# Optimization experiments

Hardware: AMD Instinct MI355X
Metric: run time of the kernel (lower is better)

Reference implementation:

```python
import jax, jax.numpy as jnp
import numpy as np

BIG = 10000000.0

def heaviside(x):
    return (jnp.tanh(BIG * x) + 1.0) * 0.5

def interception(Prec, PET, INSC):
    INSC = jnp.clip(INSC * 5.0, 0.5, 5.0)
    IMAX = jnp.maximum(jnp.minimum(INSC, PET), 0.0)
    INT = jnp.maximum(jnp.minimum(IMAX, Prec), 0.0)
    INR = jnp.maximum(Prec - INT, 0.0)
    return INT, INR

def soil_moisture_store(SMS1, SMSC):
    SMSC = jnp.clip(SMSC * 500.0, 50.0, 500.0)
    return jnp.maximum(jnp.minimum(SMS1, SMSC), 0.0)

def soil_fluxes(PET, INT, INR, COEFF, SQ, SMSC, SUB, CRAK, SMS1):
    COEFF = jnp.clip(COEFF * 400.0, 50.0, 400.0)
    SQ = jnp.clip(SQ * 6.0, 0.0, 6.0)
    SMSC = jnp.clip(SMSC * 500.0, 50.0, 500.0)
    SUB = jnp.clip(SUB, 0.0, 1.0)
    CRAK = jnp.clip(CRAK, 0.0, 1.0)
    cap = COEFF * jnp.exp(-SQ * SMS1 / SMSC)
    RMO = jnp.maximum(heaviside(cap - INR) * INR + heaviside(INR - cap) * cap, 0.0)
    IRUN = jnp.maximum(INR - RMO, 0.0)
    SRUN = jnp.maximum(SUB * (SMS1 / SMSC) * RMO, 0.0)
    REC = jnp.maximum(CRAK * (SMS1 / SMSC) * (RMO - SRUN), 0.0)
    SMF = jnp.maximum(RMO - SRUN - REC, 0.0)
    POT = jnp.maximum(PET - INT, 0.0)
    r = 10.0 * SMS1 / SMSC
    ETS = jnp.maximum(heaviside(r - POT) * POT + heaviside(POT - r) * r, 0.0)
    return RMO, IRUN, SRUN, REC, SMF, ETS

def recharge_calculation(SMS1, SMSC, REC, SMF, ETS):
    SMSC = jnp.clip(SMSC * 500.0, 50.0, 500.0)
    s = SMS1 + SMF - ETS
    RECnew = heaviside(s - SMSC) * (REC + s - SMSC) + heaviside(SMSC - s) * REC
    return jnp.maximum(RECnew, 0.0)

def groundwaterstore(GW1, RecK):
    RecK = jnp.clip(RecK * 0.3, 0.003, 0.3)
    return jnp.maximum(heaviside(GW1) * (RecK * GW1), 0.0)

def _forward(inputs, INSC, COEFF, SQ, SMSC, SUB, CRAK, RecK):
    B, T, _ = inputs.shape
    xs = jnp.transpose(inputs, (1, 0, 2))  # (T, B, 2)

    def step(carry, x):
        SMS1, GW1 = carry  # each (B, 1)
        Prec, PET = x[:, 0:1], x[:, 1:2]
        INT, INR = interception(Prec, PET, INSC)
        SMS1c = soil_moisture_store(SMS1, SMSC)
        RMO, IRUN, SRUN, REC, SMF, ETS = soil_fluxes(PET, INT, INR, COEFF, SQ, SMSC, SUB, CRAK, SMS1c)
        next_SMS = SMS1c + jnp.clip(SMF - ETS, -100000.0, 100000.0)
        RECnew = recharge_calculation(SMS1c, SMSC, REC, SMF, ETS)
        BAS = groundwaterstore(GW1, RecK)
        next_GW = GW1 + jnp.clip(RECnew - BAS, -100000.0, 100000.0)
        return (next_SMS, next_GW), jnp.concatenate([next_SMS, next_GW], axis=1)

    init = (jnp.zeros((B, 1), inputs.dtype), jnp.zeros((B, 1), inputs.dtype))
    _, outs = jax.lax.scan(step, init, xs)  # (T, B, 2)
    outs = jnp.transpose(outs, (1, 0, 2))   # (B, T, 2)
    outs = jnp.roll(outs, shift=1, axis=1)  # state at step t-1 (wrap like tf.roll)
    SMS1 = outs[:, :, 0:1]
    GW1 = outs[:, :, 1:2]
    Prec = inputs[:, :, 0:1]
    PET = inputs[:, :, 1:2]
    INT, INR = interception(Prec, PET, INSC)
    SMS1 = soil_moisture_store(SMS1, SMSC)
    RMO, IRUN, SRUN, REC, SMF, ETS = soil_fluxes(PET, INT, INR, COEFF, SQ, SMSC, SUB, CRAK, SMS1)
    RECnew = recharge_calculation(SMS1, SMSC, REC, SMF, ETS)
    BAS = groundwaterstore(GW1, RecK)
    DR = jnp.maximum(SRUN + IRUN, 0.0)
    GD = jnp.maximum(BAS, 0.0)
    Q = jnp.maximum(DR + GD, 0.0)
    return Q  # (B, T, 1)


def setup_inputs() -> dict:
    key = jax.random.key(0)
    k1, = jax.random.split(key, 1)
    B, T = 4096, 1024
    # Prec in [0, 20) mm/day, PET in [0, 8) mm/day
    u = jax.random.uniform(k1, (B, T, 2), dtype=jnp.float32)
    scale = jnp.array([20.0, 8.0], dtype=jnp.float32)
    inputs = u * scale
    p = lambda v: jnp.full((1,), v, dtype=jnp.float32)
    return {
        "inputs": inputs,
        "INSC": p(0.5), "COEFF": p(0.5), "SQ": p(0.5), "SMSC": p(0.5),
        "SUB": p(0.5), "CRAK": p(0.5), "RecK": p(0.5),
    }


def reference(inputs, INSC, COEFF, SQ, SMSC, SUB, CRAK, RecK):
    return _forward(inputs, INSC, COEFF, SQ, SMSC, SUB, CRAK, RecK)
```

## Files before the change

### kernel.cpp

```cpp
#include <hip/hip_runtime.h>
#include <hip/hip_bf16.h>
#include <math.h>


struct P {
    float INSC, COEFF, SMSC, RecK, k1, k2, k3, c2;
};

__device__ __forceinline__ P make_params(const float* pINSC, const float* pCOEFF,
                                         const float* pSQ,   const float* pSMSC,
                                         const float* pSUB,  const float* pCRAK,
                                         const float* pRecK) {
    P p;
    p.INSC  = fminf(fmaxf(pINSC[0]  * 5.0f,   0.5f),   5.0f);
    p.COEFF = fminf(fmaxf(pCOEFF[0] * 400.0f, 50.0f),  400.0f);
    float SQ = fminf(fmaxf(pSQ[0]   * 6.0f,   0.0f),   6.0f);
    p.SMSC  = fminf(fmaxf(pSMSC[0]  * 500.0f, 50.0f),  500.0f);
    float SUB  = fminf(fmaxf(pSUB[0],  0.0f), 1.0f);
    float CRAK = fminf(fmaxf(pCRAK[0], 0.0f), 1.0f);
    p.RecK  = fminf(fmaxf(pRecK[0]  * 0.3f,   0.003f), 0.3f);
    float inv = 1.0f / p.SMSC;
    p.k1 = SUB * inv;
    p.k2 = CRAK * inv;
    p.k3 = 10.0f * inv;
    p.c2 = (-SQ * inv) * 1.44269504088896340736f;
    return p;
}

__device__ __forceinline__ float step(float Prec, float PET, float& sms, float& gw, const P& p) {
    float INT   = fminf(fminf(p.INSC, PET), Prec);
    float INR   = Prec - INT;
    float POT   = PET - INT;
    float S     = fmaxf(fminf(sms, p.SMSC), 0.0f);
    float cap   = p.COEFF * exp2f(p.c2 * S);
    float RMO   = fminf(INR, cap);
    float IRUN  = INR - RMO;
    float SRUN  = (p.k1 * S) * RMO;
    float t2    = RMO - SRUN;
    float REC   = (p.k2 * S) * t2;
    float SMF   = t2 - REC;
    float ETS   = fminf(POT, p.k3 * S);
    float s2    = S + (SMF - ETS);
    float RECnew = REC + fmaxf(s2 - p.SMSC, 0.0f);
    float BAS   = p.RecK * gw;
    float Q     = (SRUN + IRUN) + BAS;
    sms = s2;
    gw  = gw + (RECnew - BAS);
    return Q;
}

__device__ __forceinline__ void stepw(float Prec, float PET, float& sms, float& gw, const P& p) {
    float INT   = fminf(fminf(p.INSC, PET), Prec);
    float INR   = Prec - INT;
    float POT   = PET - INT;
    float S     = fmaxf(fminf(sms, p.SMSC), 0.0f);
    float cap   = p.COEFF * exp2f(p.c2 * S);
    float RMO   = fminf(INR, cap);
    float SRUN  = (p.k1 * S) * RMO;
    float t2    = RMO - SRUN;
    float REC   = (p.k2 * S) * t2;
    float SMF   = t2 - REC;
    float ETS   = fminf(POT, p.k3 * S);
    float s2    = S + (SMF - ETS);
    float RECnew = REC + fmaxf(s2 - p.SMSC, 0.0f);
    float BAS   = p.RecK * gw;
    sms = s2;
    gw  = gw + (RECnew - BAS);
}

__device__ __forceinline__ void dstep(float Prec, float PET,
                                      float& slo, float& shi, float& gw, const P& p) {
    float INT = fminf(fminf(p.INSC, PET), Prec);
    float INR = Prec - INT;
    float POT = PET - INT;
    {
        float S     = fmaxf(fminf(shi, p.SMSC), 0.0f);
        float cap   = p.COEFF * exp2f(p.c2 * S);
        float RMO   = fminf(INR, cap);
        float SRUN  = (p.k1 * S) * RMO;
        float t2    = RMO - SRUN;
        float REC   = (p.k2 * S) * t2;
        float SMF   = t2 - REC;
        float ETS   = fminf(POT, p.k3 * S);
        float s2    = S + (SMF - ETS);
        float RECnew = REC + fmaxf(s2 - p.SMSC, 0.0f);
        float BAS   = p.RecK * gw;
        gw  = gw + (RECnew - BAS);
        shi = s2;
    }
    {
        float S     = fmaxf(fminf(slo, p.SMSC), 0.0f);
        float cap   = p.COEFF * exp2f(p.c2 * S);
        float RMO   = fminf(INR, cap);
        float SRUN  = (p.k1 * S) * RMO;
        float t2    = RMO - SRUN;
        float REC   = (p.k2 * S) * t2;
        float SMF   = t2 - REC;
        float ETS   = fminf(POT, p.k3 * S);
        slo = S + (SMF - ETS);
    }
}

#define MERGE_TOL 0.75f

template<int T, int NC, int W>
__global__ __launch_bounds__(64, 1)
void hir_pass1(const float* __restrict__ inputs,
               const float* __restrict__ pINSC,  const float* __restrict__ pCOEFF,
               const float* __restrict__ pSQ,    const float* __restrict__ pSMSC,
               const float* __restrict__ pSUB,   const float* __restrict__ pCRAK,
               const float* __restrict__ pRecK,
               float* __restrict__ out, float4* __restrict__ st, int B)
{
    int gid = blockIdx.x * blockDim.x + threadIdx.x;
    int b = gid % B;
    int c = gid / B;
    if (c >= NC) return;

    P p = make_params(pINSC, pCOEFF, pSQ, pSMSC, pSUB, pCRAK, pRecK);

    const float4* __restrict__ rp = (const float4*)(inputs + (size_t)b * (2 * T));
    float* __restrict__ orow = out + (size_t)b * T;

    constexpr int CH = T / NC;
    const int i1 = (c * CH) >> 1;
    const int i2 = ((c + 1) * CH) >> 1;
    int i0 = i1 - (W >> 1);
    const bool exact = (i0 <= 0);
    if (i0 < 0) i0 = 0;

    float slo = 0.0f, shi = exact ? 0.0f : p.SMSC, gw = 0.0f;

    const int nwb = (i1 - i0) >> 2;
    if (nwb > 0) {
        float4 A[4], Bq[4], C[4];
        #pragma unroll
        for (int j = 0; j < 4; ++j) A[j] = rp[i0 + j];
        {
            int k1b = (1 < nwb) ? 1 : 0;
            #pragma unroll
            for (int j = 0; j < 4; ++j) Bq[j] = rp[i0 + 4 * k1b + j];
        }
        if (exact) {
            for (int k = 0; k < nwb; ++k) {
                int kn = (k + 2 < nwb) ? (k + 2) : (nwb - 1);
                #pragma unroll
                for (int j = 0; j < 4; ++j) C[j] = rp[i0 + 4 * kn + j];
                #pragma unroll
                for (int j = 0; j < 4; ++j) {
                    stepw(A[j].x, A[j].y, shi, gw, p);
                    stepw(A[j].z, A[j].w, shi, gw, p);
                }
                #pragma unroll
                for (int j = 0; j < 4; ++j) { A[j] = Bq[j]; Bq[j] = C[j]; }
            }
            slo = shi;
        } else {
            for (int k = 0; k < nwb; ++k) {
                int kn = (k + 2 < nwb) ? (k + 2) : (nwb - 1);
                #pragma unroll
                for (int j = 0; j < 4; ++j) C[j] = rp[i0 + 4 * kn + j];
                #pragma unroll
                for (int j = 0; j < 4; ++j) {
                    dstep(A[j].x, A[j].y, slo, shi, gw, p);
                    dstep(A[j].z, A[j].w, slo, shi, gw, p);
                }
                #pragma unroll
                for (int j = 0; j < 4; ++j) { A[j] = Bq[j]; Bq[j] = C[j]; }
            }
        }
    }
    const bool merged = exact || ((shi - slo) <= MERGE_TOL);
    float sms = exact ? shi : (0.5f * (slo + shi));

    {
        constexpr int nmb = (CH / 2) / 4;
        float4 A[4], Bq[4], C[4];
        #pragma unroll
        for (int j = 0; j < 4; ++j) A[j] = rp[i1 + j];
        #pragma unroll
        for (int j = 0; j < 4; ++j) Bq[j] = rp[i1 + 4 + j];
        for (int k = 0; k < nmb; ++k) {
            int kn = (k + 2 < nmb) ? (k + 2) : (nmb - 1);
            #pragma unroll
            for (int j = 0; j < 4; ++j) C[j] = rp[i1 + 4 * kn + j];
            int ibase = i1 + 4 * k;
            #pragma unroll
            for (int j = 0; j < 4; ++j) {
                float qa = step(A[j].x, A[j].y, sms, gw, p);
                float qb = step(A[j].z, A[j].w, sms, gw, p);
                if (c == 0 && k == 0 && j == 0) {
                    orow[1] = qb;
                } else {
                    ((float2*)orow)[ibase + j] = make_float2(qa, qb);
                }
            }
            #pragma unroll
            for (int j = 0; j < 4; ++j) { A[j] = Bq[j]; Bq[j] = C[j]; }
        }
    }

    st[(size_t)c * B + b] = make_float4(sms, gw, merged ? 1.0f : 0.0f, 0.0f);

    if (c == NC - 1) {
        float4 f0 = rp[0];
        float ss = sms, gg = gw;
        orow[0] = step(f0.x, f0.y, ss, gg, p);
    }
}

template<int T, int NC>
__global__ __launch_bounds__(64, 1)
void hir_pass2(const float* __restrict__ inputs,
               const float* __restrict__ pINSC,  const float* __restrict__ pCOEFF,
               const float* __restrict__ pSQ,    const float* __restrict__ pSMSC,
               const float* __restrict__ pSUB,   const float* __restrict__ pCRAK,
               const float* __restrict__ pRecK,
               float* __restrict__ out, const float4* __restrict__ st, int B)
{
    int b = blockIdx.x * blockDim.x + threadIdx.x;
    if (b >= B) return;

    P p = make_params(pINSC, pCOEFF, pSQ, pSMSC, pSUB, pCRAK, pRecK);
    constexpr int CH = T / NC;

    const float4* __restrict__ rp = (const float4*)(inputs + (size_t)b * (2 * T));
    float* __restrict__ orow = out + (size_t)b * T;

    float4 s0 = st[b];
    float ex_s = s0.x, ex_g = s0.y;

    for (int c = 1; c < NC; ++c) {
        float4 sc = st[(size_t)c * B + b];
        if (sc.z != 0.0f) {
            ex_s = sc.x; ex_g = sc.y;
            continue;
        }
        float sms = ex_s, gw = ex_g;
        const int i1 = (c * CH) >> 1;
        const int i2 = ((c + 1) * CH) >> 1;
        float4 cur = rp[i1];
        for (int i = i1; i < i2; ++i) {
            int ni = (i + 1 < i2) ? (i + 1) : i;
            float4 nxt = rp[ni];
            float qa = step(cur.x, cur.y, sms, gw, p);
            float qb = step(cur.z, cur.w, sms, gw, p);
            ((float2*)orow)[i] = make_float2(qa, qb);
            cur = nxt;
        }
        ex_s = sms; ex_g = gw;
        if (c == NC - 1) {
            float4 f0 = rp[0];
            float ss = sms, gg = gw;
            orow[0] = step(f0.x, f0.y, ss, gg, p);
        }
    }
}

template<int T>
__global__ __launch_bounds__(64, 1)
void hir_scan_kernel(const float* __restrict__ inputs,
                     const float* __restrict__ pINSC,  const float* __restrict__ pCOEFF,
                     const float* __restrict__ pSQ,    const float* __restrict__ pSMSC,
                     const float* __restrict__ pSUB,   const float* __restrict__ pCRAK,
                     const float* __restrict__ pRecK,
                     float* __restrict__ out, int B)
{
    int b = blockIdx.x * blockDim.x + threadIdx.x;
    if (b >= B) return;
    P p = make_params(pINSC, pCOEFF, pSQ, pSMSC, pSUB, pCRAK, pRecK);
    const float4* __restrict__ rp = (const float4*)(inputs + (size_t)b * (2 * T));
    float* __restrict__ orow = out + (size_t)b * T;
    float sms = 0.0f, gw = 0.0f;
    float4 cur = rp[0];
    const float P0 = cur.x, E0 = cur.y;
    constexpr int NI = T / 2;
    for (int i = 0; i < NI; ++i) {
        int ni = (i + 1 < NI) ? (i + 1) : i;
        float4 nxt = rp[ni];
        float qa = step(cur.x, cur.y, sms, gw, p);
        float qb = step(cur.z, cur.w, sms, gw, p);
        if (i == 0) { orow[1] = qb; }
        else        { ((float2*)orow)[i] = make_float2(qa, qb); }
        cur = nxt;
    }
    float ss = sms, gg = gw;
    orow[0] = step(P0, E0, ss, gg, p);
}

extern "C" void kernel_launch(void* const* d_in, const int* in_sizes, int n_in,
                              void* d_out, int out_size, void* d_ws, size_t ws_size,
                              hipStream_t stream) {
    (void)n_in; (void)out_size;
    constexpr int T  = 1024;
    constexpr int NC = 16;
    constexpr int W  = 320;
    const float* inputs = (const float*)d_in[0];
    const float* INSC   = (const float*)d_in[1];
    const float* COEFF  = (const float*)d_in[2];
    const float* SQ     = (const float*)d_in[3];
    const float* SMSC   = (const float*)d_in[4];
    const float* SUB    = (const float*)d_in[5];
    const float* CRAK   = (const float*)d_in[6];
    const float* RecK   = (const float*)d_in[7];
    float* out = (float*)d_out;

    int B = in_sizes[0] / (2 * T);
    size_t need = (size_t)B * NC * sizeof(float4);

    if (ws_size < need || (B % 64) != 0) {
        int blocks = (B + 63) / 64;
        hir_scan_kernel<T><<<dim3(blocks), dim3(64), 0, stream>>>(
            inputs, INSC, COEFF, SQ, SMSC, SUB, CRAK, RecK, out, B);
        return;
    }

    float4* st = (float4*)d_ws;
    long total = (long)B * NC;
    int blocks1 = (int)((total + 63) / 64);
    hir_pass1<T, NC, W><<<dim3(blocks1), dim3(64), 0, stream>>>(
        inputs, INSC, COEFF, SQ, SMSC, SUB, CRAK, RecK, out, st, B);
    int blocks2 = (B + 63) / 64;
    hir_pass2<T, NC><<<dim3(blocks2), dim3(64), 0, stream>>>(
        inputs, INSC, COEFF, SQ, SMSC, SUB, CRAK, RecK, out, st, B);
}
```

Measured before the change: 134.5 us.

## Parallelize fixup pass over chunks and simplify per-step arithmetic

Pass 2 now launches one thread per (row, chunk) instead of one per row. Each unmerged chunk walks back to the nearest merged chunk's state, replays the intervening steps without writing outputs, then recomputes its own chunk. This removes the serial loop over chunks per row. The step math is also refactored: COEFF is folded into the exp2 argument via log2, the clamp-to-zero is dropped, the gw update becomes a single FMA, and several muls become FMAs. The replay can duplicate work when consecutive chunks fail to merge, and the algebraic changes may shift results slightly.

```diff
diff --git a/kernel.cpp b/kernel.cpp
--- a/kernel.cpp
+++ b/kernel.cpp
@@ -4,7 +4,7 @@
 
 
 struct P {
-    float INSC, COEFF, SMSC, RecK, k1, k2, k3, c2;
+    float INSC, SMSC, RecK, g1, lc, k1, k2, k3, c2;
 };
 
 __device__ __forceinline__ P make_params(const float* pINSC, const float* pCOEFF,
@@ -12,13 +12,15 @@
                                          const float* pSUB,  const float* pCRAK,
                                          const float* pRecK) {
     P p;
-    p.INSC  = fminf(fmaxf(pINSC[0]  * 5.0f,   0.5f),   5.0f);
-    p.COEFF = fminf(fmaxf(pCOEFF[0] * 400.0f, 50.0f),  400.0f);
-    float SQ = fminf(fmaxf(pSQ[0]   * 6.0f,   0.0f),   6.0f);
-    p.SMSC  = fminf(fmaxf(pSMSC[0]  * 500.0f, 50.0f),  500.0f);
-    float SUB  = fminf(fmaxf(pSUB[0],  0.0f), 1.0f);
-    float CRAK = fminf(fmaxf(pCRAK[0], 0.0f), 1.0f);
-    p.RecK  = fminf(fmaxf(pRecK[0]  * 0.3f,   0.003f), 0.3f);
+    p.INSC      = fminf(fmaxf(pINSC[0]  * 5.0f,   0.5f),   5.0f);
+    float COEFF = fminf(fmaxf(pCOEFF[0] * 400.0f, 50.0f),  400.0f);
+    float SQ    = fminf(fmaxf(pSQ[0]    * 6.0f,   0.0f),   6.0f);
+    p.SMSC      = fminf(fmaxf(pSMSC[0]  * 500.0f, 50.0f),  500.0f);
+    float SUB   = fminf(fmaxf(pSUB[0],  0.0f), 1.0f);
+    float CRAK  = fminf(fmaxf(pCRAK[0], 0.0f), 1.0f);
+    p.RecK      = fminf(fmaxf(pRecK[0]  * 0.3f,   0.003f), 0.3f);
+    p.g1 = 1.0f - p.RecK;
+    p.lc = log2f(COEFF);
     float inv = 1.0f / p.SMSC;
     p.k1 = SUB * inv;
     p.k2 = CRAK * inv;
@@ -28,44 +30,46 @@
 }
 
 __device__ __forceinline__ float step(float Prec, float PET, float& sms, float& gw, const P& p) {
-    float INT   = fminf(fminf(p.INSC, PET), Prec);
-    float INR   = Prec - INT;
-    float POT   = PET - INT;
-    float S     = fmaxf(fminf(sms, p.SMSC), 0.0f);
-    float cap   = p.COEFF * exp2f(p.c2 * S);
-    float RMO   = fminf(INR, cap);
-    float IRUN  = INR - RMO;
-    float SRUN  = (p.k1 * S) * RMO;
-    float t2    = RMO - SRUN;
-    float REC   = (p.k2 * S) * t2;
-    float SMF   = t2 - REC;
-    float ETS   = fminf(POT, p.k3 * S);
-    float s2    = S + (SMF - ETS);
+    float INT  = fminf(fminf(p.INSC, PET), Prec);
+    float INR  = Prec - INT;
+    float POT  = PET - INT;
+    float S    = fminf(sms, p.SMSC);
+    float u    = fmaf(-p.k1, S, 1.0f);
+    float v    = fmaf(-p.k2, S, 1.0f);
+    float ETS  = fminf(POT, p.k3 * S);
+    float SmE  = S - ETS;
+    float e    = exp2f(fmaf(p.c2, S, p.lc));
+    float RMO  = fminf(INR, e);
+    float w    = u * RMO;
+    float s2   = fmaf(v, w, SmE);
+    float SMF  = v * w;
+    float REC  = w - SMF;
     float RECnew = REC + fmaxf(s2 - p.SMSC, 0.0f);
-    float BAS   = p.RecK * gw;
-    float Q     = (SRUN + IRUN) + BAS;
+    float BAS  = p.RecK * gw;
+    float Q    = (INR - w) + BAS;
+    gw  = fmaf(p.g1, gw, RECnew);
     sms = s2;
-    gw  = gw + (RECnew - BAS);
     return Q;
 }
 
 __device__ __forceinline__ void stepw(float Prec, float PET, float& sms, float& gw, const P& p) {
-    float INT   = fminf(fminf(p.INSC, PET), Prec);
-    float INR   = Prec - INT;
-    float POT   = PET - INT;
-    float S     = fmaxf(fminf(sms, p.SMSC), 0.0f);
-    float cap   = p.COEFF * exp2f(p.c2 * S);
-    float RMO   = fminf(INR, cap);
-    float SRUN  = (p.k1 * S) * RMO;
-    float t2    = RMO - SRUN;
-    float REC   = (p.k2 * S) * t2;
-    float SMF   = t2 - REC;
-    float ETS   = fminf(POT, p.k3 * S);
-    float s2    = S + (SMF - ETS);
+    float INT  = fminf(fminf(p.INSC, PET), Prec);
+    float INR  = Prec - INT;
+    float POT  = PET - INT;
+    float S    = fminf(sms, p.SMSC);
+    float u    = fmaf(-p.k1, S, 1.0f);
+    float v    = fmaf(-p.k2, S, 1.0f);
+    float ETS  = fminf(POT, p.k3 * S);
+    float SmE  = S - ETS;
+    float e    = exp2f(fmaf(p.c2, S, p.lc));
+    float RMO  = fminf(INR, e);
+    float w    = u * RMO;
+    float s2   = fmaf(v, w, SmE);
+    float SMF  = v * w;
+    float REC  = w - SMF;
     float RECnew = REC + fmaxf(s2 - p.SMSC, 0.0f);
-    float BAS   = p.RecK * gw;
+    gw  = fmaf(p.g1, gw, RECnew);
     sms = s2;
-    gw  = gw + (RECnew - BAS);
 }
 
 __device__ __forceinline__ void dstep(float Prec, float PET,
@@ -74,30 +78,31 @@
     float INR = Prec - INT;
     float POT = PET - INT;
     {
-        float S     = fmaxf(fminf(shi, p.SMSC), 0.0f);
-        float cap   = p.COEFF * exp2f(p.c2 * S);
-        float RMO   = fminf(INR, cap);
-        float SRUN  = (p.k1 * S) * RMO;
-        float t2    = RMO - SRUN;
-        float REC   = (p.k2 * S) * t2;
-        float SMF   = t2 - REC;
-        float ETS   = fminf(POT, p.k3 * S);
-        float s2    = S + (SMF - ETS);
+        float S    = fminf(shi, p.SMSC);
+        float u    = fmaf(-p.k1, S, 1.0f);
+        float v    = fmaf(-p.k2, S, 1.0f);
+        float ETS  = fminf(POT, p.k3 * S);
+        float SmE  = S - ETS;
+        float e    = exp2f(fmaf(p.c2, S, p.lc));
+        float RMO  = fminf(INR, e);
+        float w    = u * RMO;
+        float s2   = fmaf(v, w, SmE);
+        float SMF  = v * w;
+        float REC  = w - SMF;
         float RECnew = REC + fmaxf(s2 - p.SMSC, 0.0f);
-        float BAS   = p.RecK * gw;
-        gw  = gw + (RECnew - BAS);
+        gw  = fmaf(p.g1, gw, RECnew);
         shi = s2;
     }
     {
-        float S     = fmaxf(fminf(slo, p.SMSC), 0.0f);
-        float cap   = p.COEFF * exp2f(p.c2 * S);
-        float RMO   = fminf(INR, cap);
-        float SRUN  = (p.k1 * S) * RMO;
-        float t2    = RMO - SRUN;
-        float REC   = (p.k2 * S) * t2;
-        float SMF   = t2 - REC;
-        float ETS   = fminf(POT, p.k3 * S);
-        slo = S + (SMF - ETS);
+        float S    = fminf(slo, p.SMSC);
+        float u    = fmaf(-p.k1, S, 1.0f);
+        float v    = fmaf(-p.k2, S, 1.0f);
+        float ETS  = fminf(POT, p.k3 * S);
+        float SmE  = S - ETS;
+        float e    = exp2f(fmaf(p.c2, S, p.lc));
+        float RMO  = fminf(INR, e);
+        float w    = u * RMO;
+        slo = fmaf(v, w, SmE);
     }
 }
 
@@ -124,7 +129,6 @@
 
     constexpr int CH = T / NC;
     const int i1 = (c * CH) >> 1;
-    const int i2 = ((c + 1) * CH) >> 1;
     int i0 = i1 - (W >> 1);
     const bool exact = (i0 <= 0);
     if (i0 < 0) i0 = 0;
@@ -218,8 +222,13 @@
                const float* __restrict__ pRecK,
                float* __restrict__ out, const float4* __restrict__ st, int B)
 {
-    int b = blockIdx.x * blockDim.x + threadIdx.x;
-    if (b >= B) return;
+    int gid = blockIdx.x * blockDim.x + threadIdx.x;
+    int b = gid % B;
+    int c = gid / B;
+    if (c >= NC) return;
+
+    float4 sc = st[(size_t)c * B + b];
+    if (sc.z != 0.0f) return;
 
     P p = make_params(pINSC, pCOEFF, pSQ, pSMSC, pSUB, pCRAK, pRecK);
     constexpr int CH = T / NC;
@@ -227,16 +236,27 @@
     const float4* __restrict__ rp = (const float4*)(inputs + (size_t)b * (2 * T));
     float* __restrict__ orow = out + (size_t)b * T;
 
-    float4 s0 = st[b];
-    float ex_s = s0.x, ex_g = s0.y;
-
-    for (int c = 1; c < NC; ++c) {
-        float4 sc = st[(size_t)c * B + b];
-        if (sc.z != 0.0f) {
-            ex_s = sc.x; ex_g = sc.y;
-            continue;
-        }
-        float sms = ex_s, gw = ex_g;
+    int m = c - 1;
+    float4 sm = st[(size_t)m * B + b];
+    while (sm.z == 0.0f) { --m; sm = st[(size_t)m * B + b]; }
+    float sms = sm.x, gw = sm.y;
+
+    {
+        const int ia = ((m + 1) * CH) >> 1;
+        const int ib = (c * CH) >> 1;
+        if (ia < ib) {
+            float4 cur = rp[ia];
+            for (int i = ia; i < ib; ++i) {
+                int ni = (i + 1 < ib) ? (i + 1) : i;
+                float4 nxt = rp[ni];
+                stepw(cur.x, cur.y, sms, gw, p);
+                stepw(cur.z, cur.w, sms, gw, p);
+                cur = nxt;
+            }
+        }
+    }
+
+    {
         const int i1 = (c * CH) >> 1;
         const int i2 = ((c + 1) * CH) >> 1;
         float4 cur = rp[i1];
@@ -248,12 +268,12 @@
             ((float2*)orow)[i] = make_float2(qa, qb);
             cur = nxt;
         }
-        ex_s = sms; ex_g = gw;
-        if (c == NC - 1) {
-            float4 f0 = rp[0];
-            float ss = sms, gg = gw;
-            orow[0] = step(f0.x, f0.y, ss, gg, p);
-        }
+    }
+
+    if (c == NC - 1) {
+        float4 f0 = rp[0];
+        float ss = sms, gg = gw;
+        orow[0] = step(f0.x, f0.y, ss, gg, p);
     }
 }
 
@@ -320,7 +340,7 @@
     int blocks1 = (int)((total + 63) / 64);
     hir_pass1<T, NC, W><<<dim3(blocks1), dim3(64), 0, stream>>>(
         inputs, INSC, COEFF, SQ, SMSC, SUB, CRAK, RecK, out, st, B);
-    int blocks2 = (B + 63) / 64;
+    int blocks2 = (int)((total + 63) / 64);
     hir_pass2<T, NC><<<dim3(blocks2), dim3(64), 0, stream>>>(
         inputs, INSC, COEFF, SQ, SMSC, SUB, CRAK, RecK, out, st, B);
 }
```

Result: faster. 120.8 us (-10.2%).
